# Optimization experiments

Measured on AMD Instinct MI355X. Metric: run time of the kernel, lower is better.

The kernel has to match this reference:

```python
import jax, jax.numpy as jnp
import numpy as np

N = 200000      # total nodes
E = 800000      # directed edges
G = 4096        # graphs in batch
D_DRUG = 128
D_CELL = 954
HID = 128
OUT = 128
EPS = 1e-5      # BatchNorm eps


def _bn(x, gamma, beta):
    # training-mode BatchNorm1d (batch statistics, biased var), dropout is eval/identity
    m = jnp.mean(x, axis=0)
    v = jnp.mean((x - m) ** 2, axis=0)
    return gamma * (x - m) * jax.lax.rsqrt(v + EPS) + beta


def _gcn_conv(x, edge_index, W, b):
    # PyG GCNConv: add self-loops, symmetric normalization, aggregate, then bias
    src = jnp.concatenate([edge_index[0], jnp.arange(N)])
    dst = jnp.concatenate([edge_index[1], jnp.arange(N)])
    ones = jnp.ones(src.shape[0], dtype=x.dtype)
    deg = jax.ops.segment_sum(ones, dst, num_segments=N)
    dinv = jnp.where(deg > 0, jax.lax.rsqrt(jnp.maximum(deg, 1.0)), 0.0)
    norm = dinv[src] * dinv[dst]                      # [E+N]
    h = x @ W                                         # [N, out]
    msg = h[src] * norm[:, None]                      # gather + scale
    out = jax.ops.segment_sum(msg, dst, num_segments=N)  # scatter-add
    return out + b


def setup_inputs() -> dict:
    key = jax.random.key(0)
    ks = jax.random.split(key, 12)
    x = jax.random.normal(ks[0], (N, D_DRUG), jnp.float32)
    edge_index = jax.random.randint(ks[1], (2, E), 0, N)
    ibatch = (jnp.arange(N) * G) // N  # sorted, every graph non-empty
    gexpr = jax.random.normal(ks[2], (G, D_CELL), jnp.float32)

    def w(k, shape):
        return jax.random.normal(k, shape, jnp.float32) / np.float32(np.sqrt(shape[0]))

    return {
        "x": x, "edge_index": edge_index, "ibatch": ibatch, "gexpr": gexpr,
        "W1": w(ks[3], (D_DRUG, HID)), "b1": jnp.zeros((HID,), jnp.float32),
        "g1": jnp.ones((HID,), jnp.float32), "be1": jnp.zeros((HID,), jnp.float32),
        "W2": w(ks[4], (HID, OUT)), "b2": jnp.zeros((OUT,), jnp.float32),
        "g2": jnp.ones((OUT,), jnp.float32), "be2": jnp.zeros((OUT,), jnp.float32),
        "Wc1": w(ks[5], (D_CELL, HID)), "bc1": jnp.zeros((HID,), jnp.float32),
        "gc": jnp.ones((HID,), jnp.float32), "bec": jnp.zeros((HID,), jnp.float32),
        "Wc2": w(ks[6], (HID, OUT)), "bc2": jnp.zeros((OUT,), jnp.float32),
    }


def reference(x, edge_index, ibatch, gexpr,
              W1, b1, g1, be1, W2, b2, g2, be2,
              Wc1, bc1, gc, bec, Wc2, bc2):
    # drug branch
    h = _gcn_conv(x, edge_index, W1, b1)
    h = _bn(jax.nn.relu(h), g1, be1)
    h = _gcn_conv(h, edge_index, W2, b2)
    h = _bn(jax.nn.relu(h), g2, be2)
    x_drug = jax.ops.segment_max(h, ibatch, num_segments=G)  # global_max_pool
    # cellline branch
    c = jnp.tanh(gexpr @ Wc1 + bc1)
    c = _bn(c, gc, bec)
    x_cell = jax.nn.relu(c @ Wc2 + bc2)
    return x_drug, x_cell
```

## Files before the change

### kernel.cpp

```cpp
#include <hip/hip_runtime.h>

#define NFEAT 128

typedef __attribute__((ext_vector_type(4))) float f32x4;
typedef __attribute__((ext_vector_type(8))) short bf16x8;

__device__ __forceinline__ unsigned short f2bf(float f) {
    unsigned u = __builtin_bit_cast(unsigned, f);
    u += 0x7fffu + ((u >> 16) & 1u);
    return (unsigned short)(u >> 16);
}
__device__ __forceinline__ float bf2f(unsigned short s) {
    unsigned u = ((unsigned)s) << 16;
    return __builtin_bit_cast(float, u);
}

__device__ __forceinline__ void dma16(const void* g, void* l) {
    __builtin_amdgcn_global_load_lds(
        (const __attribute__((address_space(1))) unsigned int*)g,
        (__attribute__((address_space(3))) unsigned int*)l, 16, 0, 0);
}

template <int ACT, typename OutT, typename AT>
__global__ __launch_bounds__(256) void gemm_dma(
    const AT* __restrict__ A, const unsigned short* __restrict__ Bt,
    OutT* __restrict__ C, int M, int ldA, int ldB,
    const float* __restrict__ bias, const float* __restrict__ dscale)
{
    constexpr bool AF32 = (sizeof(AT) == 4);
    __shared__ AT ash[64 * 128];
    const int tid = threadIdx.x;
    const int wv = tid >> 6, lane = tid & 63;
    const int l16 = lane & 15, quad = lane >> 4;
    const int kbase = blockIdx.y * 128;
    const long tile0 = (long)blockIdx.x * 64;

    const int nc0 = (wv & 1) * 64;
    bf16x8 bfr[4][4];
#pragma unroll
    for (int nt = 0; nt < 4; ++nt) {
        const unsigned short* bp =
            Bt + (size_t)(nc0 + nt * 16 + l16) * ldB + kbase + quad * 8;
#pragma unroll
        for (int ks = 0; ks < 4; ++ks)
            bfr[nt][ks] = *(const bf16x8*)(bp + ks * 32);
    }

    {
        const int r0 = wv * 16;
        if constexpr (AF32) {
#pragma unroll
            for (int j = 0; j < 8; ++j) {
                const float* gp = (const float*)A +
                    (size_t)(tile0 + r0 + j * 2 + (lane >> 5)) * ldA + kbase +
                    (lane & 31) * 4;
                dma16(gp, (void*)&ash[(r0 + j * 2) * 128]);
            }
        } else {
#pragma unroll
            for (int j = 0; j < 4; ++j) {
                const unsigned short* gp = (const unsigned short*)A +
                    (size_t)(tile0 + r0 + j * 4 + (lane >> 4)) * ldA + kbase +
                    l16 * 8;
                dma16(gp, (void*)&ash[(r0 + j * 4) * 128]);
            }
        }
    }
    __syncthreads();

    const int rh = wv >> 1;
    bf16x8 af[2][4];
#pragma unroll
    for (int mt = 0; mt < 2; ++mt) {
        const int row = rh * 32 + mt * 16 + l16;
#pragma unroll
        for (int ks = 0; ks < 4; ++ks) {
            if constexpr (AF32) {
                const float* lp = (const float*)&ash[0] + row * 128 + ks * 32 + quad * 8;
                f32x4 v0 = *(const f32x4*)lp;
                f32x4 v1 = *(const f32x4*)(lp + 4);
                bf16x8 t;
                t[0] = (short)f2bf(v0[0]); t[1] = (short)f2bf(v0[1]);
                t[2] = (short)f2bf(v0[2]); t[3] = (short)f2bf(v0[3]);
                t[4] = (short)f2bf(v1[0]); t[5] = (short)f2bf(v1[1]);
                t[6] = (short)f2bf(v1[2]); t[7] = (short)f2bf(v1[3]);
                af[mt][ks] = t;
            } else {
                af[mt][ks] = *(const bf16x8*)((const unsigned short*)&ash[0] +
                                              row * 128 + ks * 32 + quad * 8);
            }
        }
    }

    f32x4 acc[2][4];
#pragma unroll
    for (int a = 0; a < 2; ++a)
#pragma unroll
        for (int b = 0; b < 4; ++b) acc[a][b] = (f32x4){0.f, 0.f, 0.f, 0.f};
#pragma unroll
    for (int ks = 0; ks < 4; ++ks)
#pragma unroll
        for (int nt = 0; nt < 4; ++nt)
#pragma unroll
            for (int mt = 0; mt < 2; ++mt)
                acc[mt][nt] = __builtin_amdgcn_mfma_f32_16x16x32_bf16(
                    af[mt][ks], bfr[nt][ks], acc[mt][nt], 0, 0, 0);

    C += (size_t)blockIdx.y * M * NFEAT;
    float ds[2][4];
#pragma unroll
    for (int mt = 0; mt < 2; ++mt)
#pragma unroll
        for (int r = 0; r < 4; ++r) {
            long row = tile0 + rh * 32 + mt * 16 + quad * 4 + r;
            ds[mt][r] = dscale ? dscale[row] : 1.f;
        }
#pragma unroll
    for (int nt = 0; nt < 4; ++nt) {
        int col = nc0 + nt * 16 + l16;
        float bv = bias ? bias[col] : 0.f;
#pragma unroll
        for (int mt = 0; mt < 2; ++mt) {
            long rbase = tile0 + rh * 32 + mt * 16 + quad * 4;
#pragma unroll
            for (int r = 0; r < 4; ++r) {
                float v = acc[mt][nt][r] + bv;
                if (ACT == 1) v = tanhf(v);
                if (ACT == 2) v = fmaxf(v, 0.f);
                v *= ds[mt][r];
                if constexpr (sizeof(OutT) == 2)
                    C[(size_t)(rbase + r) * NFEAT + col] = (OutT)f2bf(v);
                else
                    C[(size_t)(rbase + r) * NFEAT + col] = (OutT)v;
            }
        }
    }
}

__global__ void k_transpose(const float* __restrict__ W, unsigned short* __restrict__ Wt,
                            int K, int Kp)
{
    int idx = blockIdx.x * 256 + threadIdx.x;
    if (idx >= 128 * Kp) return;
    int n = idx / Kp, k = idx - n * Kp;
    Wt[idx] = (k < K) ? f2bf(W[(size_t)k * NFEAT + n]) : (unsigned short)0;
}

__global__ void k_bnfold_w(const float* __restrict__ sums8, const float* __restrict__ gamma,
                           const float* __restrict__ beta, float invN,
                           const float* __restrict__ W, const float* __restrict__ extra,
                           unsigned short* __restrict__ Wt, float* __restrict__ brow)
{
    __shared__ float ssc[128], ssh[128];
    int t = threadIdx.x;
    if (t < 128) {
        float s = 0.f, s2 = 0.f;
#pragma unroll
        for (int c = 0; c < 8; ++c) { s += sums8[c * 256 + t]; s2 += sums8[c * 256 + 128 + t]; }
        float mean = s * invN;
        float var = s2 * invN - mean * mean;
        float rstd = rsqrtf(fmaxf(var, 0.f) + 1e-5f);
        float sc = gamma[t] * rstd;
        ssc[t] = sc;
        ssh[t] = beta[t] - mean * sc;
    }
    __syncthreads();
    if (blockIdx.x < 64) {
        int idx = blockIdx.x * 256 + t;
        int n = idx >> 7, k = idx & 127;
        Wt[idx] = f2bf(W[(size_t)k * NFEAT + n] * ssc[k]);
    } else if (t < 128) {
        float s = extra ? extra[t] : 0.f;
        for (int k = 0; k < 128; ++k) s += ssh[k] * W[(size_t)k * NFEAT + t];
        brow[t] = s;
    }
}

__global__ void k_finalize8(const float* __restrict__ sums8, const float* __restrict__ gamma,
                            const float* __restrict__ beta, float* __restrict__ scale,
                            float* __restrict__ shift, float invN)
{
    int j = threadIdx.x;
    float s = 0.f, s2 = 0.f;
#pragma unroll
    for (int c = 0; c < 8; ++c) { s += sums8[c * 256 + j]; s2 += sums8[c * 256 + 128 + j]; }
    float mean = s * invN;
    float var = s2 * invN - mean * mean;
    float rstd = rsqrtf(fmaxf(var, 0.f) + 1e-5f);
    float sc = gamma[j] * rstd;
    scale[j] = sc;
    shift[j] = beta[j] - mean * sc;
}

__global__ void k_padA(const float* __restrict__ g, float* __restrict__ Ap,
                       int G, int DC, int DCP)
{
    long idx = (long)blockIdx.x * 256 + threadIdx.x;
    if (idx >= (long)G * DCP) return;
    long i = idx / DCP; int k = (int)(idx - i * DCP);
    Ap[idx] = (k < DC) ? g[i * DC + k] : 0.f;
}

__global__ void k_degi(const int* __restrict__ dst, int* __restrict__ deg, int E)
{
    int e = blockIdx.x * 256 + threadIdx.x;
    if (e < E) atomicAdd(&deg[dst[e]], 1);
}

__global__ __launch_bounds__(256) void k_scan1(const int* __restrict__ deg,
        int* __restrict__ rowptr, int* __restrict__ bsum, float* __restrict__ dinv, int N)
{
    __shared__ int sh[256];
    int t = threadIdx.x;
    int base = blockIdx.x * 1024 + t * 4;
    int v[4];
#pragma unroll
    for (int j = 0; j < 4; ++j) {
        v[j] = (base + j < N) ? deg[base + j] : 0;
        if (base + j < N) dinv[base + j] = rsqrtf((float)(v[j] + 1));
    }
    int s = v[0] + v[1] + v[2] + v[3];
    sh[t] = s;
    __syncthreads();
    int incl = s;
    for (int off = 1; off < 256; off <<= 1) {
        int x = (t >= off) ? sh[t - off] : 0;
        __syncthreads();
        incl += x;
        sh[t] = incl;
        __syncthreads();
    }
    int run = incl - s;
#pragma unroll
    for (int j = 0; j < 4; ++j) {
        if (base + j < N) rowptr[base + j] = run;
        run += v[j];
    }
    if (t == 255) bsum[blockIdx.x] = incl;
}

__global__ void k_scan2(int* __restrict__ bsum, int nb)
{
    __shared__ int sh[256];
    int t = threadIdx.x;
    int s = (t < nb) ? bsum[t] : 0;
    sh[t] = s;
    __syncthreads();
    int incl = s;
    for (int off = 1; off < 256; off <<= 1) {
        int x = (t >= off) ? sh[t - off] : 0;
        __syncthreads();
        incl += x;
        sh[t] = incl;
        __syncthreads();
    }
    if (t < nb) bsum[t] = incl - s;
}

__global__ void k_scan3(int* __restrict__ rowptr, int* __restrict__ cursor,
                        const int* __restrict__ bsum, int N, int E)
{
    int i = blockIdx.x * 256 + threadIdx.x;
    if (i < N) {
        int v = rowptr[i] + bsum[i >> 10];
        rowptr[i] = v;
        cursor[i] = v;
    } else if (i == N) {
        rowptr[N] = E;
    }
}

__global__ void k_fill(const int* __restrict__ src, const int* __restrict__ dst,
                       int* __restrict__ cursor, int* __restrict__ csr, int E)
{
    int e = blockIdx.x * 256 + threadIdx.x;
    if (e < E) {
        int pos = atomicAdd(&cursor[dst[e]], 1);
        csr[pos] = src[e];
    }
}

__device__ __forceinline__ void unpack_add(float* acc, uint4 a)
{
    acc[0] += bf2f((unsigned short)(a.x & 0xffff));
    acc[1] += bf2f((unsigned short)(a.x >> 16));
    acc[2] += bf2f((unsigned short)(a.y & 0xffff));
    acc[3] += bf2f((unsigned short)(a.y >> 16));
    acc[4] += bf2f((unsigned short)(a.z & 0xffff));
    acc[5] += bf2f((unsigned short)(a.z >> 16));
    acc[6] += bf2f((unsigned short)(a.w & 0xffff));
    acc[7] += bf2f((unsigned short)(a.w >> 16));
}

__global__ __launch_bounds__(256) void k_agg(
    const unsigned short* __restrict__ h, const int* __restrict__ rowptr,
    const int* __restrict__ csr, const float* __restrict__ dinv,
    const float* __restrict__ bias, unsigned short* __restrict__ out,
    float* __restrict__ sums8, int N)
{
    __shared__ float red[4][256];
    const int tid = threadIdx.x;
    const int wv = tid >> 6, lane = tid & 63;
    const int f = (tid & 15) << 3;
    const long g0 = (long)blockIdx.x * 16 + (tid >> 4);
    const long gstride = (long)gridDim.x * 16;

    f32x4 b0 = *(const f32x4*)&bias[f];
    f32x4 b1 = *(const f32x4*)&bias[f + 4];

    float s8[8], q8[8];
#pragma unroll
    for (int j = 0; j < 8; ++j) { s8[j] = 0.f; q8[j] = 0.f; }

    for (long i = g0; i < N; i += gstride) {
        float acc[8];
#pragma unroll
        for (int j = 0; j < 8; ++j) acc[j] = 0.f;

        int lo = rowptr[i], hi = rowptr[i + 1];
        int e = lo;
        for (; e + 3 < hi; e += 4) {
            int s0 = csr[e], s1 = csr[e + 1], s2 = csr[e + 2], s3 = csr[e + 3];
            uint4 a = *(const uint4*)(h + ((size_t)s0 << 7) + f);
            uint4 b = *(const uint4*)(h + ((size_t)s1 << 7) + f);
            uint4 c = *(const uint4*)(h + ((size_t)s2 << 7) + f);
            uint4 d = *(const uint4*)(h + ((size_t)s3 << 7) + f);
            unpack_add(acc, a); unpack_add(acc, b);
            unpack_add(acc, c); unpack_add(acc, d);
        }
        for (; e < hi; ++e) {
            int s0 = csr[e];
            uint4 a = *(const uint4*)(h + ((size_t)s0 << 7) + f);
            unpack_add(acc, a);
        }
        uint4 hs = *(const uint4*)(h + ((size_t)i << 7) + f);
        unpack_add(acc, hs);

        float di = dinv[i];
        unsigned short o[8];
#pragma unroll
        for (int j = 0; j < 8; ++j) {
            float bj = (j < 4) ? b0[j] : b1[j - 4];
            float v = fmaxf(di * acc[j] + bj, 0.f);
            o[j] = f2bf(v);
            s8[j] += v; q8[j] += v * v;
        }
        *(uint4*)(out + (i << 7) + f) = *(const uint4*)o;
    }

#pragma unroll
    for (int j = 0; j < 8; ++j) {
        s8[j] += __shfl_xor(s8[j], 16);
        s8[j] += __shfl_xor(s8[j], 32);
        q8[j] += __shfl_xor(q8[j], 16);
        q8[j] += __shfl_xor(q8[j], 32);
    }
    if (lane < 16) {
#pragma unroll
        for (int j = 0; j < 8; ++j) {
            red[wv][f + j] = s8[j];
            red[wv][128 + f + j] = q8[j];
        }
    }
    __syncthreads();
    float tot = red[0][tid] + red[1][tid] + red[2][tid] + red[3][tid];
    atomicAdd(&sums8[(blockIdx.x & 7) * 256 + tid], tot);
}

__global__ void k_cellred(const float* __restrict__ p, const float* __restrict__ bias,
                          unsigned short* __restrict__ cbuf, float* __restrict__ sums8, int G)
{
    int j = threadIdx.x & 127;
    int slot = blockIdx.x * 2 + (threadIdx.x >> 7);
    int nslots = gridDim.x * 2;
    const size_t st = (size_t)G * NFEAT;
    float b = bias[j], s = 0.f, s2 = 0.f;
    for (int i = slot; i < G; i += nslots) {
        size_t o = (size_t)i * NFEAT + j;
        float v = b;
#pragma unroll
        for (int c = 0; c < 8; ++c) v += p[o + c * st];
        v = tanhf(v);
        cbuf[o] = f2bf(v);
        s += v; s2 += v * v;
    }
    atomicAdd(&sums8[(blockIdx.x & 7) * 256 + j], s);
    atomicAdd(&sums8[(blockIdx.x & 7) * 256 + 128 + j], s2);
}

__global__ void k_segmax(const unsigned short* __restrict__ agg, const float* __restrict__ scale,
                         const float* __restrict__ shift, float* __restrict__ out,
                         int N, int G)
{
    int g = blockIdx.x;
    int j = threadIdx.x;
    int lo = (int)(((long long)g * N + G - 1) / G);
    int hi = (int)(((long long)(g + 1) * N + G - 1) / G);
    float sc = scale[j], sh = shift[j];
    float m = -INFINITY;
    for (int i = lo; i < hi; ++i)
        m = fmaxf(m, bf2f(agg[(size_t)i * NFEAT + j]) * sc + sh);
    out[(size_t)g * NFEAT + j] = m;
}

extern "C" void kernel_launch(void* const* d_in, const int* in_sizes, int n_in,
                              void* d_out, int out_size, void* d_ws, size_t ws_size,
                              hipStream_t stream)
{
    const float* x     = (const float*)d_in[0];
    const int*   ei    = (const int*)d_in[1];
    const float* gexpr = (const float*)d_in[3];
    const float* W1  = (const float*)d_in[4];
    const float* b1  = (const float*)d_in[5];
    const float* g1  = (const float*)d_in[6];
    const float* be1 = (const float*)d_in[7];
    const float* W2  = (const float*)d_in[8];
    const float* b2  = (const float*)d_in[9];
    const float* g2  = (const float*)d_in[10];
    const float* be2 = (const float*)d_in[11];
    const float* Wc1 = (const float*)d_in[12];
    const float* bc1 = (const float*)d_in[13];
    const float* gc  = (const float*)d_in[14];
    const float* bec = (const float*)d_in[15];
    const float* Wc2 = (const float*)d_in[16];
    const float* bc2 = (const float*)d_in[17];

    const int N = in_sizes[0] / NFEAT;
    const int E = in_sizes[1] / 2;
    const int G = in_sizes[3] / 954;
    const int DC = 954, DCP = 1024;

    char* wsp = (char*)d_ws;
    size_t off = 0;
    auto alloc = [&](size_t bytes) -> char* {
        char* p = wsp + off;
        off += (bytes + 255) & ~(size_t)255;
        return p;
    };
    unsigned short* agg    = (unsigned short*)alloc((size_t)N * NFEAT * 2);
    unsigned short* h      = (unsigned short*)alloc((size_t)N * NFEAT * 2);
    float*          dinv   = (float*)alloc((size_t)N * 4);
    int*            deg    = (int*)alloc((size_t)N * 4);
    int*            rowptr = (int*)alloc((size_t)(N + 1) * 4);
    int*            cursor = (int*)alloc((size_t)N * 4);
    int*            csr    = (int*)alloc((size_t)E * 4);
    int*            bsum   = (int*)alloc(256 * 4);
    float*          Apad   = (float*)alloc((size_t)G * DCP * 4);
    float*          pbuf   = (float*)alloc((size_t)8 * G * NFEAT * 4);
    unsigned short* cbuf   = (unsigned short*)alloc((size_t)G * NFEAT * 2);
    unsigned short* W1t    = (unsigned short*)alloc(128 * 128 * 2);
    unsigned short* W2t    = (unsigned short*)alloc(128 * 128 * 2);
    unsigned short* Wc1t   = (unsigned short*)alloc(128 * DCP * 2);
    unsigned short* Wc2t   = (unsigned short*)alloc(128 * 128 * 2);
    float*          stats  = (float*)alloc(8192 * 4);
    float* sums1 = stats,         * sums2 = stats + 2048, * sumsC = stats + 4096;
    float* scale2 = stats + 6144, * shift2 = stats + 6272;
    float* brow2  = stats + 6400, * browC  = stats + 6528;

    hipMemsetAsync(stats, 0, 6144 * 4, stream);
    hipMemsetAsync(deg, 0, (size_t)N * 4, stream);

    const int* esrc = ei;
    const int* edst = ei + E;

    k_transpose<<<(128 * 128 + 255) / 256, 256, 0, stream>>>(W1, W1t, 128, 128);
    k_transpose<<<(128 * DCP + 255) / 256, 256, 0, stream>>>(Wc1, Wc1t, DC, DCP);
    k_padA<<<(int)(((long)G * DCP + 255) / 256), 256, 0, stream>>>(gexpr, Apad, G, DC, DCP);

    const int nb = (N + 1023) / 1024;
    k_degi<<<(E + 255) / 256, 256, 0, stream>>>(edst, deg, E);
    k_scan1<<<nb, 256, 0, stream>>>(deg, rowptr, bsum, dinv, N);
    k_scan2<<<1, 256, 0, stream>>>(bsum, nb);
    k_scan3<<<(N + 1 + 255) / 256, 256, 0, stream>>>(rowptr, cursor, bsum, N, E);
    k_fill<<<(E + 255) / 256, 256, 0, stream>>>(esrc, edst, cursor, csr, E);

    const int gtiles = N / 64;
    const int ablocks = 2048;

    gemm_dma<0, unsigned short, float><<<dim3(gtiles, 1), 256, 0, stream>>>(
        x, W1t, h, N, 128, 128, nullptr, dinv);
    k_agg<<<ablocks, 256, 0, stream>>>(h, rowptr, csr, dinv, b1, agg, sums1, N);

    k_bnfold_w<<<65, 256, 0, stream>>>(sums1, g1, be1, 1.f / (float)N, W2, nullptr, W2t, brow2);
    gemm_dma<0, unsigned short, unsigned short><<<dim3(gtiles, 1), 256, 0, stream>>>(
        agg, W2t, h, N, 128, 128, brow2, dinv);
    k_agg<<<ablocks, 256, 0, stream>>>(h, rowptr, csr, dinv, b2, agg, sums2, N);
    k_finalize8<<<1, 128, 0, stream>>>(sums2, g2, be2, scale2, shift2, 1.f / (float)N);

    float* outp = (float*)d_out;
    k_segmax<<<G, 128, 0, stream>>>(agg, scale2, shift2, outp, N, G);

    gemm_dma<0, float, float><<<dim3(G / 64, 8), 256, 0, stream>>>(
        Apad, Wc1t, pbuf, G, DCP, DCP, nullptr, nullptr);
    k_cellred<<<32, 256, 0, stream>>>(pbuf, bc1, cbuf, sumsC, G);
    k_bnfold_w<<<65, 256, 0, stream>>>(sumsC, gc, bec, 1.f / (float)G, Wc2, bc2, Wc2t, browC);
    gemm_dma<2, float, unsigned short><<<dim3(G / 64, 1), 256, 0, stream>>>(
        cbuf, Wc2t, outp + (size_t)G * NFEAT, G, 128, 128, browC, nullptr);
}
```

Baseline: 526.1 us.

## Fuse second aggregation with global max pool via per-graph max/min tracking

The second GCN aggregation now keeps per-graph running max and min of the post-ReLU values in shared memory instead of writing the full bf16 node feature matrix. A small apply kernel then picks max or min depending on the sign of the BN scale, which removes the node-feature write and the separate segmax pass over it. The gather loop is also restructured to issue six predicated neighbour loads up front, using a zero padding row in h so short rows need no branches. Occupancy is hinted with launch bounds and the block count is lowered to 1536. The fused version relies on each block covering at most three graphs and uses many LDS atomics per node.

```diff
diff --git a/kernel.cpp b/kernel.cpp
--- a/kernel.cpp
+++ b/kernel.cpp
@@ -292,7 +292,41 @@
     acc[7] += bf2f((unsigned short)(a.w >> 16));
 }
 
-__global__ __launch_bounds__(256) void k_agg(
+__device__ __forceinline__ void row_gather(const unsigned short* __restrict__ h,
+    const int* __restrict__ rowptr, const int* __restrict__ csr,
+    long i, int f, int N, float* acc)
+{
+    int lo = rowptr[i], hi = rowptr[i + 1];
+    int n = hi - lo;
+    int idx[6];
+#pragma unroll
+    for (int j = 0; j < 6; ++j) {
+        int cv = csr[lo + j];
+        idx[j] = (j < n) ? cv : N;
+    }
+    uint4 ga[6];
+#pragma unroll
+    for (int j = 0; j < 6; ++j)
+        ga[j] = *(const uint4*)(h + ((size_t)idx[j] << 7) + f);
+    uint4 gs = *(const uint4*)(h + ((size_t)i << 7) + f);
+#pragma unroll
+    for (int j = 0; j < 6; ++j) unpack_add(acc, ga[j]);
+    unpack_add(acc, gs);
+    if (n > 6) {
+        int e = lo + 6;
+        for (; e + 1 < hi; e += 2) {
+            uint4 a = *(const uint4*)(h + ((size_t)csr[e] << 7) + f);
+            uint4 b = *(const uint4*)(h + ((size_t)csr[e + 1] << 7) + f);
+            unpack_add(acc, a); unpack_add(acc, b);
+        }
+        if (e < hi) {
+            uint4 a = *(const uint4*)(h + ((size_t)csr[e] << 7) + f);
+            unpack_add(acc, a);
+        }
+    }
+}
+
+__global__ __launch_bounds__(256, 6) void k_agg(
     const unsigned short* __restrict__ h, const int* __restrict__ rowptr,
     const int* __restrict__ csr, const float* __restrict__ dinv,
     const float* __restrict__ bias, unsigned short* __restrict__ out,
@@ -316,25 +350,7 @@
         float acc[8];
 #pragma unroll
         for (int j = 0; j < 8; ++j) acc[j] = 0.f;
-
-        int lo = rowptr[i], hi = rowptr[i + 1];
-        int e = lo;
-        for (; e + 3 < hi; e += 4) {
-            int s0 = csr[e], s1 = csr[e + 1], s2 = csr[e + 2], s3 = csr[e + 3];
-            uint4 a = *(const uint4*)(h + ((size_t)s0 << 7) + f);
-            uint4 b = *(const uint4*)(h + ((size_t)s1 << 7) + f);
-            uint4 c = *(const uint4*)(h + ((size_t)s2 << 7) + f);
-            uint4 d = *(const uint4*)(h + ((size_t)s3 << 7) + f);
-            unpack_add(acc, a); unpack_add(acc, b);
-            unpack_add(acc, c); unpack_add(acc, d);
-        }
-        for (; e < hi; ++e) {
-            int s0 = csr[e];
-            uint4 a = *(const uint4*)(h + ((size_t)s0 << 7) + f);
-            unpack_add(acc, a);
-        }
-        uint4 hs = *(const uint4*)(h + ((size_t)i << 7) + f);
-        unpack_add(acc, hs);
+        row_gather(h, rowptr, csr, i, f, N, acc);
 
         float di = dinv[i];
         unsigned short o[8];
@@ -365,6 +381,99 @@
     __syncthreads();
     float tot = red[0][tid] + red[1][tid] + red[2][tid] + red[3][tid];
     atomicAdd(&sums8[(blockIdx.x & 7) * 256 + tid], tot);
+}
+
+__global__ __launch_bounds__(256, 6) void k_aggmax(
+    const unsigned short* __restrict__ h, const int* __restrict__ rowptr,
+    const int* __restrict__ csr, const float* __restrict__ dinv,
+    const float* __restrict__ bias, int* __restrict__ gmax, int* __restrict__ gmin,
+    float* __restrict__ sums8, int N, int G, int NB)
+{
+    __shared__ float red[4][256];
+    __shared__ int lmax[3][128], lmin[3][128];
+    const int tid = threadIdx.x;
+    const int wv = tid >> 6, lane = tid & 63;
+    const int f = (tid & 15) << 3;
+    const int grp = tid >> 4;
+    const int b = blockIdx.x;
+    const int g_lo = (int)(((long long)b * G) / NB);
+    const int g_hi = (int)(((long long)(b + 1) * G) / NB);
+    const int ngr = g_hi - g_lo;
+    const int rstart = (int)(((long long)g_lo * N + G - 1) / G);
+    const int rend   = (int)(((long long)g_hi * N + G - 1) / G);
+    const int bnd1   = (int)(((long long)(g_lo + 1) * N + G - 1) / G);
+    const int bnd2   = (ngr >= 3) ? (int)(((long long)(g_lo + 2) * N + G - 1) / G)
+                                  : rend;
+
+    for (int idx = tid; idx < 3 * 128; idx += 256) {
+        ((int*)lmax)[idx] = 0;
+        ((int*)lmin)[idx] = 0x7f800000;
+    }
+    __syncthreads();
+
+    f32x4 b0 = *(const f32x4*)&bias[f];
+    f32x4 b1 = *(const f32x4*)&bias[f + 4];
+
+    float s8[8], q8[8];
+#pragma unroll
+    for (int j = 0; j < 8; ++j) { s8[j] = 0.f; q8[j] = 0.f; }
+
+    for (long i = rstart + grp; i < rend; i += 16) {
+        float acc[8];
+#pragma unroll
+        for (int j = 0; j < 8; ++j) acc[j] = 0.f;
+        row_gather(h, rowptr, csr, i, f, N, acc);
+
+        float di = dinv[i];
+        int gi = (i >= bnd1) + (i >= bnd2);
+        int* lmx = &lmax[gi][f];
+        int* lmn = &lmin[gi][f];
+#pragma unroll
+        for (int j = 0; j < 8; ++j) {
+            float bj = (j < 4) ? b0[j] : b1[j - 4];
+            float v = fmaxf(di * acc[j] + bj, 0.f);
+            s8[j] += v; q8[j] += v * v;
+            int bits = __builtin_bit_cast(int, v);
+            atomicMax(&lmx[j], bits);
+            atomicMin(&lmn[j], bits);
+        }
+    }
+
+#pragma unroll
+    for (int j = 0; j < 8; ++j) {
+        s8[j] += __shfl_xor(s8[j], 16);
+        s8[j] += __shfl_xor(s8[j], 32);
+        q8[j] += __shfl_xor(q8[j], 16);
+        q8[j] += __shfl_xor(q8[j], 32);
+    }
+    if (lane < 16) {
+#pragma unroll
+        for (int j = 0; j < 8; ++j) {
+            red[wv][f + j] = s8[j];
+            red[wv][128 + f + j] = q8[j];
+        }
+    }
+    __syncthreads();
+    float tot = red[0][tid] + red[1][tid] + red[2][tid] + red[3][tid];
+    atomicAdd(&sums8[(blockIdx.x & 7) * 256 + tid], tot);
+
+    for (int idx = tid; idx < ngr * 128; idx += 256) {
+        int gg = idx >> 7, j = idx & 127;
+        gmax[(size_t)(g_lo + gg) * 128 + j] = lmax[gg][j];
+        gmin[(size_t)(g_lo + gg) * 128 + j] = lmin[gg][j];
+    }
+}
+
+__global__ void k_segapply(const int* __restrict__ gmax, const int* __restrict__ gmin,
+                           const float* __restrict__ scale, const float* __restrict__ shift,
+                           float* __restrict__ out, int total)
+{
+    int idx = blockIdx.x * 256 + threadIdx.x;
+    if (idx >= total) return;
+    int j = idx & 127;
+    float sc = scale[j], sh = shift[j];
+    int bits = (sc >= 0.f) ? gmax[idx] : gmin[idx];
+    out[idx] = sc * __builtin_bit_cast(float, bits) + sh;
 }
 
 __global__ void k_cellred(const float* __restrict__ p, const float* __restrict__ bias,
@@ -386,21 +495,6 @@
     }
     atomicAdd(&sums8[(blockIdx.x & 7) * 256 + j], s);
     atomicAdd(&sums8[(blockIdx.x & 7) * 256 + 128 + j], s2);
-}
-
-__global__ void k_segmax(const unsigned short* __restrict__ agg, const float* __restrict__ scale,
-                         const float* __restrict__ shift, float* __restrict__ out,
-                         int N, int G)
-{
-    int g = blockIdx.x;
-    int j = threadIdx.x;
-    int lo = (int)(((long long)g * N + G - 1) / G);
-    int hi = (int)(((long long)(g + 1) * N + G - 1) / G);
-    float sc = scale[j], sh = shift[j];
-    float m = -INFINITY;
-    for (int i = lo; i < hi; ++i)
-        m = fmaxf(m, bf2f(agg[(size_t)i * NFEAT + j]) * sc + sh);
-    out[(size_t)g * NFEAT + j] = m;
 }
 
 extern "C" void kernel_launch(void* const* d_in, const int* in_sizes, int n_in,
@@ -438,16 +532,18 @@
         return p;
     };
     unsigned short* agg    = (unsigned short*)alloc((size_t)N * NFEAT * 2);
-    unsigned short* h      = (unsigned short*)alloc((size_t)N * NFEAT * 2);
+    unsigned short* h      = (unsigned short*)alloc((size_t)(N + 1) * NFEAT * 2);
     float*          dinv   = (float*)alloc((size_t)N * 4);
     int*            deg    = (int*)alloc((size_t)N * 4);
     int*            rowptr = (int*)alloc((size_t)(N + 1) * 4);
     int*            cursor = (int*)alloc((size_t)N * 4);
-    int*            csr    = (int*)alloc((size_t)E * 4);
+    int*            csr    = (int*)alloc((size_t)(E + 8) * 4);
     int*            bsum   = (int*)alloc(256 * 4);
     float*          Apad   = (float*)alloc((size_t)G * DCP * 4);
     float*          pbuf   = (float*)alloc((size_t)8 * G * NFEAT * 4);
     unsigned short* cbuf   = (unsigned short*)alloc((size_t)G * NFEAT * 2);
+    int*            gmax   = (int*)alloc((size_t)G * NFEAT * 4);
+    int*            gmin   = (int*)alloc((size_t)G * NFEAT * 4);
     unsigned short* W1t    = (unsigned short*)alloc(128 * 128 * 2);
     unsigned short* W2t    = (unsigned short*)alloc(128 * 128 * 2);
     unsigned short* Wc1t   = (unsigned short*)alloc(128 * DCP * 2);
@@ -459,6 +555,7 @@
 
     hipMemsetAsync(stats, 0, 6144 * 4, stream);
     hipMemsetAsync(deg, 0, (size_t)N * 4, stream);
+    hipMemsetAsync(h + (size_t)N * NFEAT, 0, NFEAT * 2, stream);
 
     const int* esrc = ei;
     const int* edst = ei + E;
@@ -475,7 +572,8 @@
     k_fill<<<(E + 255) / 256, 256, 0, stream>>>(esrc, edst, cursor, csr, E);
 
     const int gtiles = N / 64;
-    const int ablocks = 2048;
+    const int ablocks = 1536;
+    const int NB = 1536;
 
     gemm_dma<0, unsigned short, float><<<dim3(gtiles, 1), 256, 0, stream>>>(
         x, W1t, h, N, 128, 128, nullptr, dinv);
@@ -484,11 +582,13 @@
     k_bnfold_w<<<65, 256, 0, stream>>>(sums1, g1, be1, 1.f / (float)N, W2, nullptr, W2t, brow2);
     gemm_dma<0, unsigned short, unsigned short><<<dim3(gtiles, 1), 256, 0, stream>>>(
         agg, W2t, h, N, 128, 128, brow2, dinv);
-    k_agg<<<ablocks, 256, 0, stream>>>(h, rowptr, csr, dinv, b2, agg, sums2, N);
+
+    k_aggmax<<<NB, 256, 0, stream>>>(h, rowptr, csr, dinv, b2, gmax, gmin, sums2, N, G, NB);
     k_finalize8<<<1, 128, 0, stream>>>(sums2, g2, be2, scale2, shift2, 1.f / (float)N);
 
     float* outp = (float*)d_out;
-    k_segmax<<<G, 128, 0, stream>>>(agg, scale2, shift2, outp, N, G);
+    k_segapply<<<(G * NFEAT + 255) / 256, 256, 0, stream>>>(
+        gmax, gmin, scale2, shift2, outp, G * NFEAT);
 
     gemm_dma<0, float, float><<<dim3(G / 64, 8), 256, 0, stream>>>(
         Apad, Wc1t, pbuf, G, DCP, DCP, nullptr, nullptr);
```

Measured after the change: 539.0 us. 1.02x slower.
